# Optimization experiments

Measured on AMD Instinct MI355X. Metric: run time of the kernel, lower is better.

The kernel has to match this reference:

```python
import jax, jax.numpy as jnp
import numpy as np

D_MODEL = 1024
N_HEADS = 16
D_HEAD = D_MODEL // N_HEADS


def setup_inputs() -> dict:
    key = jax.random.key(0)
    ks = jax.random.split(key, 5)
    s_in = 1.0 / np.sqrt(D_MODEL)
    x = jax.random.normal(ks[0], (2, 2048, D_MODEL), dtype=jnp.float32)
    W_qkv = jax.random.uniform(ks[1], (D_MODEL, 3 * D_MODEL), jnp.float32, -s_in, s_in)
    b_qkv = jax.random.uniform(ks[2], (3 * D_MODEL,), jnp.float32, -s_in, s_in)
    W_out = jax.random.uniform(ks[3], (D_MODEL, D_MODEL), jnp.float32, -s_in, s_in)
    b_out = jax.random.uniform(ks[4], (D_MODEL,), jnp.float32, -s_in, s_in)
    return {"x": x, "W_qkv": W_qkv, "b_qkv": b_qkv, "W_out": W_out, "b_out": b_out}


def reference(x, W_qkv, b_qkv, W_out, b_out):
    B, T, C = x.shape
    qkv = x @ W_qkv + b_qkv                      # [B,T,3C]
    q, k, v = jnp.split(qkv, 3, axis=-1)
    # [B,T,C] -> [B,H,T,Dh]
    def heads(t):
        return t.reshape(B, T, N_HEADS, D_HEAD).transpose(0, 2, 1, 3)
    q, k, v = heads(q), heads(k), heads(v)
    att = jnp.einsum('bhqd,bhkd->bhqk', q, k) / np.sqrt(D_HEAD).astype(np.float32)
    causal = jnp.tril(jnp.ones((T, T), dtype=bool))  # True = keep
    att = jnp.where(causal, att, -jnp.inf)
    att = jax.nn.softmax(att, axis=-1)
    y = jnp.einsum('bhqk,bhkd->bhqd', att, v)    # [B,H,T,Dh]
    y = y.transpose(0, 2, 1, 3).reshape(B, T, C)
    y = y @ W_out + b_out
    return (y, att)
```

## Files before the change

### kernel.cpp

```cpp
#include <hip/hip_runtime.h>

#define B_ 2
#define T_ 2048
#define C_ 1024
#define H_ 16
#define DH_ 64
#define N3_ 3072
#define BT_ 4096

typedef __attribute__((ext_vector_type(4))) float f32x4;
typedef __attribute__((ext_vector_type(8))) short short8;
typedef __attribute__((ext_vector_type(4))) unsigned short us4;
typedef __attribute__((ext_vector_type(4))) unsigned int u32x4;

__device__ __forceinline__ unsigned short f2bf(float f) {
  return __builtin_bit_cast(unsigned short, (__bf16)f);
}

__device__ __forceinline__ float bf2f(unsigned short s) {
  unsigned int u = ((unsigned int)s) << 16;
  return __builtin_bit_cast(float, u);
}

__device__ __forceinline__ unsigned int cvtpk(float a, float b) {
  unsigned int r;
  asm("v_cvt_pk_bf16_f32 %0, %1, %2" : "=v"(r) : "v"(a), "v"(b));
  return r;
}

__device__ __forceinline__ void gload16(const void* g, void* l) {
  __builtin_amdgcn_global_load_lds(
      (const __attribute__((address_space(1))) unsigned int*)g,
      (__attribute__((address_space(3))) unsigned int*)l, 16, 0, 0);
}

__device__ __forceinline__ void lds_barrier() {
  asm volatile("s_waitcnt lgkmcnt(0)" ::: "memory");
  __builtin_amdgcn_s_barrier();
}

#define QSCALE 0.1803368801111137f

__global__ __launch_bounds__(256) void prep_kernel(const float* __restrict__ x,
                                                   const float* __restrict__ W_qkv,
                                                   const float* __restrict__ W_out,
                                                   unsigned short* __restrict__ xb,
                                                   unsigned short* __restrict__ wqkvT,
                                                   unsigned short* __restrict__ woutT) {
  __shared__ float tile[32][33];
  int b = blockIdx.x;
  if (b < 4096) {
    size_t i = (size_t)b * 256 + threadIdx.x;
    float4 v = *(const float4*)(x + i * 4);
    us4 o = {f2bf(v.x), f2bf(v.y), f2bf(v.z), f2bf(v.w)};
    *(us4*)(xb + i * 4) = o;
    return;
  }
  const float* W;
  unsigned short* Wt;
  int Ncols, bx, by;
  if (b < 4096 + 3072) {
    int bb = b - 4096;
    W = W_qkv; Wt = wqkvT; Ncols = 3072; bx = bb % 96; by = bb / 96;
  } else {
    int bb = b - 7168;
    W = W_out; Wt = woutT; Ncols = 1024; bx = bb % 32; by = bb / 32;
  }
  int n0 = bx * 32, k0 = by * 32;
  int tx = threadIdx.x & 31, ty = threadIdx.x >> 5;
#pragma unroll
  for (int i = 0; i < 4; ++i) {
    int k = k0 + ty + i * 8;
    tile[ty + i * 8][tx] = W[(size_t)k * Ncols + n0 + tx];
  }
  __syncthreads();
#pragma unroll
  for (int i = 0; i < 4; ++i) {
    int n = n0 + ty + i * 8;
    Wt[(size_t)n * 1024 + k0 + tx] = f2bf(tile[tx][ty + i * 8]);
  }
}

template <int MODE, int BN>
__global__ __launch_bounds__(256) void gemm_kernel(
    const unsigned short* __restrict__ A, const unsigned short* __restrict__ Bt,
    const float* __restrict__ bias, unsigned short* __restrict__ q_ws,
    unsigned short* __restrict__ k_ws, unsigned short* __restrict__ vt_ws,
    float* __restrict__ yout) {
  __shared__ unsigned short lds_a[128 * 32];
  __shared__ unsigned short lds_b[BN * 32];
  const int tid = threadIdx.x;
  const int w = tid >> 6, l = tid & 63;
  const int m0 = blockIdx.y * 128;
  const int n0 = blockIdx.x * BN;
  const int wr = (w >> 1) * 64, wc = (w & 1) * (BN / 2);
  constexpr int NI = BN / 32;
  const int K = 1024;

  f32x4 acc[4][NI] = {};
  for (int k0 = 0; k0 < K; k0 += 32) {
    __syncthreads();
#pragma unroll
    for (int i = 0; i < 2; ++i) {
      int li = i * 256 + tid;
      int row = li >> 2, cl = li & 3, cs = cl ^ (row & 3);
      gload16((const char*)A + ((size_t)(m0 + row) * K + k0) * 2 + cs * 16,
              (char*)lds_a + li * 16);
    }
#pragma unroll
    for (int i = 0; i < BN / 64; ++i) {
      int li = i * 256 + tid;
      int row = li >> 2, cl = li & 3, cs = cl ^ (row & 3);
      gload16((const char*)Bt + ((size_t)(n0 + row) * K + k0) * 2 + cs * 16,
              (char*)lds_b + li * 16);
    }
    __syncthreads();
    short8 af[4], bfr[NI];
#pragma unroll
    for (int mi = 0; mi < 4; ++mi) {
      int m = wr + mi * 16 + (l & 15);
      af[mi] = *(const short8*)((const char*)lds_a + m * 64 + (((l >> 4) ^ (m & 3)) * 16));
    }
#pragma unroll
    for (int ni = 0; ni < NI; ++ni) {
      int n = wc + ni * 16 + (l & 15);
      bfr[ni] = *(const short8*)((const char*)lds_b + n * 64 + (((l >> 4) ^ (n & 3)) * 16));
    }
#pragma unroll
    for (int mi = 0; mi < 4; ++mi)
#pragma unroll
      for (int ni = 0; ni < NI; ++ni)
        acc[mi][ni] = __builtin_amdgcn_mfma_f32_16x16x32_bf16(af[mi], bfr[ni], acc[mi][ni], 0, 0, 0);
  }

  float bi[NI];
#pragma unroll
  for (int ni = 0; ni < NI; ++ni) bi[ni] = bias[n0 + wc + ni * 16 + (l & 15)];

  if (MODE == 1) {
#pragma unroll
    for (int mi = 0; mi < 4; ++mi) {
#pragma unroll
      for (int ni = 0; ni < NI; ++ni) {
        int n = n0 + wc + ni * 16 + (l & 15);
#pragma unroll
        for (int r = 0; r < 4; ++r) {
          int m = m0 + wr + mi * 16 + ((l >> 4) << 2) + r;
          yout[(size_t)m * 1024 + n] = acc[mi][ni][r] + bi[ni];
        }
      }
    }
  } else {
    int sec = (n0 + wc) >> 10;
#pragma unroll
    for (int mi = 0; mi < 4; ++mi) {
#pragma unroll
      for (int ni = 0; ni < NI; ++ni) {
        int n = n0 + wc + ni * 16 + (l & 15);
        int nn = n & 1023, h = nn >> 6, d = nn & 63;
        if (sec == 2) {
          int mbase = m0 + wr + mi * 16 + ((l >> 4) << 2);
          int bb = mbase >> 11, t = mbase & 2047;
          us4 o;
#pragma unroll
          for (int r = 0; r < 4; ++r) o[r] = f2bf(acc[mi][ni][r] + bi[ni]);
          *(us4*)(vt_ws + ((size_t)(bb * 16 + h) * 64 + d) * 2048 + t) = o;
        } else {
#pragma unroll
          for (int r = 0; r < 4; ++r) {
            int m = m0 + wr + mi * 16 + ((l >> 4) << 2) + r;
            int bb = m >> 11, t = m & 2047;
            float v = acc[mi][ni][r] + bi[ni];
            size_t idx = ((size_t)(bb * 16 + h) * 2048 + t) * 64 + d;
            if (sec == 0)
              q_ws[idx] = f2bf(v * QSCALE);
            else
              k_ws[idx] = f2bf(v);
          }
        }
      }
    }
  }
}

__global__ __launch_bounds__(512) void attn_kernel(
    const unsigned short* __restrict__ q_ws, const unsigned short* __restrict__ k_ws,
    const unsigned short* __restrict__ vt_ws, float* __restrict__ att,
    unsigned short* __restrict__ yh) {
  __shared__ unsigned short lds_k[64 * 64];
  __shared__ unsigned short lds_v[64 * 64];
  const int tid = threadIdx.x, w = tid >> 6, l = tid & 63;
  const int id = blockIdx.x;
  const int rr = id >> 8, j = id & 255;
  int qt = j & 15;
  if (rr) qt = 15 - qt;
  const int bh = (j >> 4) + (rr << 4);
  const int q0 = qt * 128;
  const size_t hoff = (size_t)bh * (2048 * 64);
  const char* kbase = (const char*)k_ws + hoff * 2;
  const char* vbase = (const char*)vt_ws + hoff * 2;

  auto stageK = [&](int kt) {
    int row = tid >> 3, cl = tid & 7, cs = cl ^ (row & 7);
    gload16(kbase + (size_t)kt * 8192 + row * 128 + cs * 16, (char*)lds_k + tid * 16);
  };
  auto stageV = [&](int kt) {
    int row = tid >> 3, cl = tid & 7, cs = cl ^ (row & 7);
    gload16(vbase + (size_t)row * 4096 + kt * 128 + cs * 16, (char*)lds_v + tid * 16);
  };

  short8 qf[2];
  {
    int row = q0 + w * 16 + (l & 15);
    const char* qb = (const char*)q_ws + (hoff + (size_t)row * 64) * 2;
    qf[0] = *(const short8*)(qb + ((l >> 4) * 16));
    qf[1] = *(const short8*)(qb + 64 + ((l >> 4) * 16));
  }

  const int qrow = q0 + w * 16 + (l & 15);
  const int kcolbase = (l >> 4) << 2;

  float lsum = 0.f;
  auto step1 = [&](int kt, bool diag) {
    lds_barrier();
    stageK(kt);
    __syncthreads();
    f32x4 s[4] = {};
#pragma unroll
    for (int ni = 0; ni < 4; ++ni) {
      int jj = ni * 16 + (l & 15);
#pragma unroll
      for (int cc = 0; cc < 2; ++cc) {
        short8 kf = *(const short8*)((const char*)lds_k + jj * 128 +
                                     (((cc * 4 + (l >> 4)) ^ (jj & 7)) * 16));
        s[ni] = __builtin_amdgcn_mfma_f32_16x16x32_bf16(kf, qf[cc], s[ni], 0, 0, 0);
      }
    }
#pragma unroll
    for (int ni = 0; ni < 4; ++ni) {
#pragma unroll
      for (int r = 0; r < 4; ++r) {
        float e = __builtin_exp2f(s[ni][r]);
        if (diag) {
          int colg = kt * 64 + ni * 16 + kcolbase + r;
          if (colg > qrow) e = 0.f;
        }
        lsum += e;
      }
    }
  };
  for (int kt = 0; kt < 2 * qt; ++kt) step1(kt, false);
  step1(2 * qt, true);
  step1(2 * qt + 1, true);

  lsum += __shfl_xor(lsum, 16);
  lsum += __shfl_xor(lsum, 32);
  const float invl = 1.0f / lsum;

  f32x4 yacc[4] = {};
  float* attb = att + (size_t)bh * 2048 * 2048;
  const int srcA = (l & 15) + ((l >> 4) & 1) * 32;
  const int srcB = srcA + 16;
  const bool hiSel = ((l >> 4) >> 1) & 1;

  auto step2 = [&](int kt, bool diag) {
    lds_barrier();
    stageK(kt);
    stageV(kt);
    __syncthreads();
    f32x4 s[4] = {};
#pragma unroll
    for (int ni = 0; ni < 4; ++ni) {
      int jj = ni * 16 + (l & 15);
#pragma unroll
      for (int cc = 0; cc < 2; ++cc) {
        short8 kf = *(const short8*)((const char*)lds_k + jj * 128 +
                                     (((cc * 4 + (l >> 4)) ^ (jj & 7)) * 16));
        s[ni] = __builtin_amdgcn_mfma_f32_16x16x32_bf16(kf, qf[cc], s[ni], 0, 0, 0);
      }
    }
    unsigned int W0[4], W1[4];
#pragma unroll
    for (int ni = 0; ni < 4; ++ni) {
      f32x4 p;
#pragma unroll
      for (int r = 0; r < 4; ++r) {
        float v = __builtin_exp2f(s[ni][r]) * invl;
        if (diag) {
          int colg = kt * 64 + ni * 16 + kcolbase + r;
          if (colg > qrow) v = 0.f;
        }
        p[r] = v;
      }
      *(f32x4*)(attb + (size_t)qrow * 2048 + kt * 64 + ni * 16 + kcolbase) = p;
      W0[ni] = cvtpk(p[0], p[1]);
      W1[ni] = cvtpk(p[2], p[3]);
    }
#pragma unroll
    for (int kk = 0; kk < 2; ++kk) {
      unsigned int a0 = __shfl(W0[2 * kk], srcA), a0b = __shfl(W0[2 * kk + 1], srcA);
      unsigned int a1 = __shfl(W1[2 * kk], srcA), a1b = __shfl(W1[2 * kk + 1], srcA);
      unsigned int b0 = __shfl(W0[2 * kk], srcB), b0b = __shfl(W0[2 * kk + 1], srcB);
      unsigned int b1 = __shfl(W1[2 * kk], srcB), b1b = __shfl(W1[2 * kk + 1], srcB);
      u32x4 F = {hiSel ? a0b : a0, hiSel ? a1b : a1, hiSel ? b0b : b0, hiSel ? b1b : b1};
      short8 pf = __builtin_bit_cast(short8, F);
#pragma unroll
      for (int ni = 0; ni < 4; ++ni) {
        int d = ni * 16 + (l & 15);
        short8 vf = *(const short8*)((const char*)lds_v + d * 128 +
                                     (((kk * 4 + (l >> 4)) ^ (d & 7)) * 16));
        yacc[ni] = __builtin_amdgcn_mfma_f32_16x16x32_bf16(pf, vf, yacc[ni], 0, 0, 0);
      }
    }
  };
  for (int kt = 0; kt < 2 * qt; ++kt) step2(kt, false);
  step2(2 * qt, true);
  step2(2 * qt + 1, true);

  {
    int bb = bh >> 4, h = bh & 15;
#pragma unroll
    for (int ni = 0; ni < 4; ++ni) {
      int d = ni * 16 + (l & 15);
#pragma unroll
      for (int r = 0; r < 4; ++r) {
        int t = q0 + w * 16 + ((l >> 4) << 2) + r;
        yh[((size_t)bb * 2048 + t) * 1024 + h * 64 + d] = f2bf(yacc[ni][r]);
      }
    }
  }

  int cstart = q0 + 128;
  if (cstart < 2048) {
    int nz = 2048 - cstart;
    float4 z = make_float4(0.f, 0.f, 0.f, 0.f);
    for (int row = 0; row < 128; ++row) {
      float* dst = attb + (size_t)(q0 + row) * 2048 + cstart;
      for (int c = tid * 4; c < nz; c += 2048) *(float4*)(dst + c) = z;
    }
  }
}

extern "C" void kernel_launch(void* const* d_in, const int* in_sizes, int n_in,
                              void* d_out, int out_size, void* d_ws, size_t ws_size,
                              hipStream_t stream) {
  const float* x = (const float*)d_in[0];
  const float* W_qkv = (const float*)d_in[1];
  const float* b_qkv = (const float*)d_in[2];
  const float* W_out = (const float*)d_in[3];
  const float* b_out = (const float*)d_in[4];
  float* out = (float*)d_out;

  char* ws = (char*)d_ws;
  unsigned short* xb = (unsigned short*)(ws);
  unsigned short* wqkvT = (unsigned short*)(ws + 8388608);
  unsigned short* woutT = (unsigned short*)(ws + 14680064);
  unsigned short* q_ws = (unsigned short*)(ws + 16777216);
  unsigned short* k_ws = (unsigned short*)(ws + 25165824);
  unsigned short* vt_ws = (unsigned short*)(ws + 33554432);
  unsigned short* yh_ws = (unsigned short*)(ws + 41943040);

  float* y_out = out;
  float* att_out = out + (size_t)BT_ * C_;

  prep_kernel<<<8192, 256, 0, stream>>>(x, W_qkv, W_out, xb, wqkvT, woutT);
  gemm_kernel<0, 128><<<dim3(24, 32), 256, 0, stream>>>(xb, wqkvT, b_qkv, q_ws, k_ws, vt_ws,
                                                        nullptr);
  attn_kernel<<<512, 512, 0, stream>>>(q_ws, k_ws, vt_ws, att_out, yh_ws);
  gemm_kernel<1, 64><<<dim3(16, 32), 256, 0, stream>>>(yh_ws, woutT, b_out, nullptr, nullptr,
                                                       nullptr, y_out);
}
```

Measured before the change: 242.7 us.

## Double-buffer K/V LDS tiles in attention to prefetch the next tile during compute

Splits the K and V LDS buffers into two halves. Each loop iteration now issues the global-to-LDS loads for the next key tile before computing on the current one, in both the row-sum pass and the output pass. The old pattern of barrier, load and barrier before every tile is replaced by a single vmcnt wait plus barrier at the end of each iteration. This aims to hide K/V load latency behind the MFMA and exp work, at the cost of twice the LDS and a vmcnt(4) wait that depends on the att stores being counted after the loads.

```diff
diff --git a/kernel.cpp b/kernel.cpp
--- a/kernel.cpp
+++ b/kernel.cpp
@@ -32,11 +32,6 @@
   __builtin_amdgcn_global_load_lds(
       (const __attribute__((address_space(1))) unsigned int*)g,
       (__attribute__((address_space(3))) unsigned int*)l, 16, 0, 0);
-}
-
-__device__ __forceinline__ void lds_barrier() {
-  asm volatile("s_waitcnt lgkmcnt(0)" ::: "memory");
-  __builtin_amdgcn_s_barrier();
 }
 
 #define QSCALE 0.1803368801111137f
@@ -187,8 +182,8 @@
     const unsigned short* __restrict__ q_ws, const unsigned short* __restrict__ k_ws,
     const unsigned short* __restrict__ vt_ws, float* __restrict__ att,
     unsigned short* __restrict__ yh) {
-  __shared__ unsigned short lds_k[64 * 64];
-  __shared__ unsigned short lds_v[64 * 64];
+  __shared__ unsigned short lds_k[2][64 * 64];
+  __shared__ unsigned short lds_v[2][64 * 64];
   const int tid = threadIdx.x, w = tid >> 6, l = tid & 63;
   const int id = blockIdx.x;
   const int rr = id >> 8, j = id & 255;
@@ -199,14 +194,15 @@
   const size_t hoff = (size_t)bh * (2048 * 64);
   const char* kbase = (const char*)k_ws + hoff * 2;
   const char* vbase = (const char*)vt_ws + hoff * 2;
-
-  auto stageK = [&](int kt) {
+  float* attb = att + (size_t)bh * 2048 * 2048;
+
+  auto stageK = [&](int kt, int buf) {
     int row = tid >> 3, cl = tid & 7, cs = cl ^ (row & 7);
-    gload16(kbase + (size_t)kt * 8192 + row * 128 + cs * 16, (char*)lds_k + tid * 16);
+    gload16(kbase + (size_t)kt * 8192 + row * 128 + cs * 16, (char*)lds_k[buf] + tid * 16);
   };
-  auto stageV = [&](int kt) {
+  auto stageV = [&](int kt, int buf) {
     int row = tid >> 3, cl = tid & 7, cs = cl ^ (row & 7);
-    gload16(vbase + (size_t)row * 4096 + kt * 128 + cs * 16, (char*)lds_v + tid * 16);
+    gload16(vbase + (size_t)row * 4096 + kt * 128 + cs * 16, (char*)lds_v[buf] + tid * 16);
   };
 
   short8 qf[2];
@@ -219,19 +215,23 @@
 
   const int qrow = q0 + w * 16 + (l & 15);
   const int kcolbase = (l >> 4) << 2;
+  const int nkt = 2 * qt + 2;
 
   float lsum = 0.f;
-  auto step1 = [&](int kt, bool diag) {
-    lds_barrier();
-    stageK(kt);
-    __syncthreads();
+  stageK(0, 0);
+  asm volatile("s_waitcnt vmcnt(0)" ::: "memory");
+  __builtin_amdgcn_s_barrier();
+  for (int kt = 0; kt < nkt; ++kt) {
+    const int cur = kt & 1;
+    if (kt + 1 < nkt) stageK(kt + 1, cur ^ 1);
+    const bool diag = (kt >= 2 * qt);
     f32x4 s[4] = {};
 #pragma unroll
     for (int ni = 0; ni < 4; ++ni) {
       int jj = ni * 16 + (l & 15);
 #pragma unroll
       for (int cc = 0; cc < 2; ++cc) {
-        short8 kf = *(const short8*)((const char*)lds_k + jj * 128 +
+        short8 kf = *(const short8*)((const char*)lds_k[cur] + jj * 128 +
                                      (((cc * 4 + (l >> 4)) ^ (jj & 7)) * 16));
         s[ni] = __builtin_amdgcn_mfma_f32_16x16x32_bf16(kf, qf[cc], s[ni], 0, 0, 0);
       }
@@ -248,33 +248,36 @@
         lsum += e;
       }
     }
-  };
-  for (int kt = 0; kt < 2 * qt; ++kt) step1(kt, false);
-  step1(2 * qt, true);
-  step1(2 * qt + 1, true);
+    if (kt + 1 < nkt) {
+      asm volatile("s_waitcnt vmcnt(0)" ::: "memory");
+      __builtin_amdgcn_s_barrier();
+    }
+  }
 
   lsum += __shfl_xor(lsum, 16);
   lsum += __shfl_xor(lsum, 32);
   const float invl = 1.0f / lsum;
 
   f32x4 yacc[4] = {};
-  float* attb = att + (size_t)bh * 2048 * 2048;
   const int srcA = (l & 15) + ((l >> 4) & 1) * 32;
   const int srcB = srcA + 16;
   const bool hiSel = ((l >> 4) >> 1) & 1;
 
-  auto step2 = [&](int kt, bool diag) {
-    lds_barrier();
-    stageK(kt);
-    stageV(kt);
-    __syncthreads();
+  stageK(0, 0);
+  stageV(0, 0);
+  asm volatile("s_waitcnt vmcnt(0)" ::: "memory");
+  __builtin_amdgcn_s_barrier();
+  for (int kt = 0; kt < nkt; ++kt) {
+    const int cur = kt & 1;
+    if (kt + 1 < nkt) { stageK(kt + 1, cur ^ 1); stageV(kt + 1, cur ^ 1); }
+    const bool diag = (kt >= 2 * qt);
     f32x4 s[4] = {};
 #pragma unroll
     for (int ni = 0; ni < 4; ++ni) {
       int jj = ni * 16 + (l & 15);
 #pragma unroll
       for (int cc = 0; cc < 2; ++cc) {
-        short8 kf = *(const short8*)((const char*)lds_k + jj * 128 +
+        short8 kf = *(const short8*)((const char*)lds_k[cur] + jj * 128 +
                                      (((cc * 4 + (l >> 4)) ^ (jj & 7)) * 16));
         s[ni] = __builtin_amdgcn_mfma_f32_16x16x32_bf16(kf, qf[cc], s[ni], 0, 0, 0);
       }
@@ -307,15 +310,16 @@
 #pragma unroll
       for (int ni = 0; ni < 4; ++ni) {
         int d = ni * 16 + (l & 15);
-        short8 vf = *(const short8*)((const char*)lds_v + d * 128 +
+        short8 vf = *(const short8*)((const char*)lds_v[cur] + d * 128 +
                                      (((kk * 4 + (l >> 4)) ^ (d & 7)) * 16));
         yacc[ni] = __builtin_amdgcn_mfma_f32_16x16x32_bf16(pf, vf, yacc[ni], 0, 0, 0);
       }
     }
-  };
-  for (int kt = 0; kt < 2 * qt; ++kt) step2(kt, false);
-  step2(2 * qt, true);
-  step2(2 * qt + 1, true);
+    if (kt + 1 < nkt) {
+      asm volatile("s_waitcnt vmcnt(4)" ::: "memory");
+      __builtin_amdgcn_s_barrier();
+    }
+  }
 
   {
     int bb = bh >> 4, h = bh & 15;
```

Result: no change. 239.4 us (-1.4%).
